# Optimization experiments

Measured on AMD Instinct MI355X. Metric: run time of the kernel, lower is better.

## Reference

```python
import jax, jax.numpy as jnp
import numpy as np

PATCH = 16
CH = 3


def setup_inputs() -> dict:
    key = jax.random.key(0)
    k1, k2, k3 = jax.random.split(key, 3)
    B, H = 16, 512
    embed_dim = PATCH * PATCH * CH  # 768
    x = jax.random.normal(k1, (B, CH, H, H), dtype=jnp.float32)
    fan_in = CH * PATCH * PATCH
    w = jax.random.normal(k2, (embed_dim, CH, PATCH, PATCH), dtype=jnp.float32) / np.float32(np.sqrt(fan_in))
    b = jax.random.normal(k3, (embed_dim,), dtype=jnp.float32) * 0.01
    return {"x": x, "w": w, "b": b}


def reference(x, w, b):
    p = w.shape[2]                      # patch_size
    B, C, imgsize, _ = x.shape
    pn = imgsize // p                   # patch_num (NOTE: pre-padding count, as in source)
    # zero-pad by one patch on every side
    xp = jnp.pad(x, ((0, 0), (0, 0), (p, p), (p, p)))
    # strided patch-embed conv: [B, embed_dim, pn+2, pn+2]
    xt = jax.lax.conv_general_dilated(xp, w, window_strides=(p, p), padding='VALID')
    xt = xt + b[None, :, None, None]
    B1, C1, H1, W1 = xt.shape           # H1 = W1 = pn + 2
    xt = xt.reshape(B1, C1, H1 * W1)
    # same (buggy-looking but faithful) index set / stride-pn neighbors as the source
    idxs = jnp.array([i * pn + j for i in range(1, pn - 1) for j in range(1, pn)], dtype=jnp.int32)
    inv8 = jnp.float32(1.0 / 8.0)

    def body(buf, idx):
        # torch aliases x_final=x_temp, so reads see earlier in-place writes -> sequential scan
        s = (buf[:, :, idx - pn] + buf[:, :, idx + pn]
             + buf[:, :, idx - 1] + buf[:, :, idx + 1]
             + buf[:, :, idx - pn - 1] + buf[:, :, idx - pn + 1]
             + buf[:, :, idx + pn - 1] + buf[:, :, idx + pn + 1]) * inv8
        return buf.at[:, :, idx].set(s), None

    xf, _ = jax.lax.scan(body, xt, idxs)
    side = imgsize + 2 * p              # embed_dim*H1*W1 == C*side*side by construction
    out = xf.reshape(B1, C, side, side)
    return out[:, :, p:imgsize + p, p:imgsize + p]
```

## Files before the change

### kernel.cpp

```cpp
#include <hip/hip_runtime.h>
#include <hip/hip_bf16.h>


typedef __attribute__((ext_vector_type(8))) short s8v;
typedef __attribute__((ext_vector_type(4))) float f4v;
typedef __attribute__((ext_vector_type(8))) unsigned short us8;
typedef __attribute__((ext_vector_type(4))) unsigned short us4;

__device__ __forceinline__ unsigned short f2bf(float f) {
    __hip_bfloat16 h = __float2bfloat16(f);
    return *reinterpret_cast<unsigned short*>(&h);
}
__device__ __forceinline__ float bf2f(unsigned short u) {
    union { unsigned int i; float f; } c; c.i = (unsigned int)u << 16; return c.f;
}

__device__ __forceinline__ void gload_lds16(const void* g, void* l) {
    __builtin_amdgcn_global_load_lds(
        (const __attribute__((address_space(1))) unsigned int*)g,
        (__attribute__((address_space(3))) unsigned int*)l,
        16, 0, 0);
}

__global__ __launch_bounds__(256) void prep_w_k(const float* __restrict__ w,
                                                unsigned short* __restrict__ w_bf) {
    int g = blockIdx.x * 256 + threadIdx.x;
    int f = g << 3;
    const float4 v0 = *(const float4*)(w + f);
    const float4 v1 = *(const float4*)(w + f + 4);
    us8 u;
    u[0] = f2bf(v0.x); u[1] = f2bf(v0.y); u[2] = f2bf(v0.z); u[3] = f2bf(v0.w);
    u[4] = f2bf(v1.x); u[5] = f2bf(v1.y); u[6] = f2bf(v1.z); u[7] = f2bf(v1.w);
    *(us8*)(w_bf + f) = u;
}

__global__ __launch_bounds__(256) void conv_gemm_fused_k(const float* __restrict__ x,
                                                         const unsigned short* __restrict__ W,
                                                         const float* __restrict__ bias,
                                                         unsigned short* __restrict__ xt) {
    __shared__ __align__(16) unsigned short As[2][128 * 32];
    __shared__ __align__(16) unsigned short Bs[2][128 * 32];
    const int tid  = threadIdx.x;
    const int lane = tid & 63, wv = tid >> 6;
    const int wr = wv >> 1, wc = wv & 1;
    const int m0 = blockIdx.x << 7, n0 = blockIdx.y << 7;

    f4v acc[4][4] = {};

    const int bb  = m0 >> 10;
    const int ph0 = (m0 >> 5) & 31;
    const int h_l = tid >> 5, pw = tid & 31;
    const int ph_l = h_l >> 1, py_l = h_l & 1;
    const int arow = (ph_l << 5) + pw;
    const int axr  = (arow >> 1) & 3;
    const int aoff0 = arow * 32 + ((( py_l << 1)      ^ axr) << 3);
    const int aoff1 = arow * 32 + ((((py_l << 1) | 1) ^ axr) << 3);
    const float* asrc = x + (size_t)bb * 786432
                          + ((ph0 + ph_l) * 16 + py_l) * 512 + (pw << 4);
    float4 ar0, ar1, ar2, ar3;
    auto loadA = [&](int k0) {
        const float* s = asrc + (k0 >> 8) * 262144 + ((k0 >> 4) & 15) * 512;
        ar0 = *(const float4*)(s);      ar1 = *(const float4*)(s + 4);
        ar2 = *(const float4*)(s + 8);  ar3 = *(const float4*)(s + 12);
    };
    auto writeA = [&](int buf) {
        us8 lo, hi;
        lo[0]=f2bf(ar0.x); lo[1]=f2bf(ar0.y); lo[2]=f2bf(ar0.z); lo[3]=f2bf(ar0.w);
        lo[4]=f2bf(ar1.x); lo[5]=f2bf(ar1.y); lo[6]=f2bf(ar1.z); lo[7]=f2bf(ar1.w);
        hi[0]=f2bf(ar2.x); hi[1]=f2bf(ar2.y); hi[2]=f2bf(ar2.z); hi[3]=f2bf(ar2.w);
        hi[4]=f2bf(ar3.x); hi[5]=f2bf(ar3.y); hi[6]=f2bf(ar3.z); hi[7]=f2bf(ar3.w);
        *(us8*)(As[buf] + aoff0) = lo;
        *(us8*)(As[buf] + aoff1) = hi;
    };

    const int l2 = lane >> 2;
    const int kx = ((lane & 3) ^ ((l2 >> 1) & 3)) << 3;
    const unsigned short* gB = W + (size_t)(n0 + (wv << 5) + l2) * 768 + kx;
    auto stageB = [&](int buf, int k0) {
        gload_lds16(gB + k0,            Bs[buf] + (wv << 10));
        gload_lds16(gB + k0 + 16 * 768, Bs[buf] + (wv << 10) + 512);
    };

    stageB(0, 0);
    loadA(0);
    writeA(0);
    __syncthreads();

    const int cq = lane >> 4;
    int cur = 0;
    for (int t = 0; t < 24; ++t) {
        if (t < 23) { stageB(cur ^ 1, (t + 1) << 5); loadA((t + 1) << 5); }
        s8v a[4], b[4];
        #pragma unroll
        for (int mi = 0; mi < 4; ++mi) {
            int ra = (wr << 6) + (mi << 4) + (lane & 15);
            a[mi] = *(const s8v*)(As[cur] + (ra << 5) + ((cq ^ ((ra >> 1) & 3)) << 3));
        }
        #pragma unroll
        for (int ni = 0; ni < 4; ++ni) {
            int rb = (wc << 6) + (ni << 4) + (lane & 15);
            b[ni] = *(const s8v*)(Bs[cur] + (rb << 5) + ((cq ^ ((rb >> 1) & 3)) << 3));
        }
        #pragma unroll
        for (int mi = 0; mi < 4; ++mi)
            #pragma unroll
            for (int ni = 0; ni < 4; ++ni)
                acc[mi][ni] = __builtin_amdgcn_mfma_f32_16x16x32_bf16(a[mi], b[ni], acc[mi][ni], 0, 0, 0);
        if (t < 23) writeA(cur ^ 1);
        __syncthreads();
        cur ^= 1;
    }

    #pragma unroll
    for (int mi = 0; mi < 4; ++mi) {
        int m  = m0 + (wr << 6) + (mi << 4) + ((lane >> 4) << 2);
        int ph = (m >> 5) & 31, pwm = m & 31;
        unsigned short* dst = xt + (((size_t)bb * 768) << 10) + (ph << 5) + pwm;
        #pragma unroll
        for (int ni = 0; ni < 4; ++ni) {
            int n = n0 + (wc << 6) + (ni << 4) + (lane & 15);
            float bv = bias[n];
            us4 o;
            o[0] = f2bf(acc[mi][ni][0] + bv);
            o[1] = f2bf(acc[mi][ni][1] + bv);
            o[2] = f2bf(acc[mi][ni][2] + bv);
            o[3] = f2bf(acc[mi][ni][3] + bv);
            *(us4*)(dst + ((size_t)n << 10)) = o;
        }
    }
}

__global__ __launch_bounds__(256) void scan_emit_k(const unsigned short* __restrict__ xt,
                                                   const float* __restrict__ bias,
                                                   float* __restrict__ out) {
    const int grp = (blockIdx.x * 256 + threadIdx.x) >> 5;
    const int j   = threadIdx.x & 31;
    const int b   = grp / 768;
    const int c1  = grp - b * 768;
    const unsigned short* basep = xt + ((size_t)grp << 10);
    float* outb = out + (size_t)b * 786432;
    const int fl0 = c1 * 1156;
    const float bias_c = bias[c1];

    auto emit = [&](int fl, float v) {
        unsigned int c   = (fl >= 591872) ? 2u : (fl >= 295936 ? 1u : 0u);
        unsigned int rem = (unsigned int)fl - c * 295936u;
        unsigned int y   = rem / 544u;
        unsigned int xx  = rem - y * 544u;
        if (y >= 16u && y < 528u && xx >= 16u && xx < 528u)
            outb[(size_t)c * 262144 + (y - 16) * 512 + (xx - 16)] = v;
    };
    auto sel = [&](int p) -> float {
        unsigned int h = (unsigned int)p / 34u;
        unsigned int w = (unsigned int)p - h * 34u;
        if ((h == 0u) | (h == 33u) | (w == 0u) | (w == 33u)) return bias_c;
        return bf2f(basep[(h - 1u) * 32u + (w - 1u)]);
    };

    float co = sel( 32 + j);
    float no = sel( 64 + j);
    float o2 = sel( 96 + j);
    float o3 = sel(128 + j);
    emit(fl0 + j, bias_c);
    float pn   = bias_c;
    float po_h = bias_c;

    for (int i = 1; i <= 30; ++i) {
        float ld = sel((i + 4) * 32 + j);
        float co_head = __shfl(co, 0, 32);
        float no_head = __shfl(no, 0, 32);
        float n2_head = __shfl(o2, 0, 32);
        float UL = __shfl_up(pn, 1, 32);   if (j == 1)  UL = po_h;
        float U  = pn;
        float UR = __shfl_down(pn, 1, 32); if (j == 31) UR = co_head;
        float Rr = __shfl_down(co, 1, 32); if (j == 31) Rr = no_head;
        float D1 = __shfl_up(no, 1, 32);
        float D2 = no;
        float D3 = __shfl_down(no, 1, 32); if (j == 31) D3 = n2_head;
        float bv = (((UL + U) + (UR + Rr)) + ((D1 + D2) + D3)) * 0.125f;
        if (j == 1) bv += co_head * 0.125f;
        float t;
        t = __shfl_up(bv, 1, 32);  bv += (j > 1) ? 0.125f * t : 0.f;
        t = __shfl_up(bv, 2, 32);  bv += (j > 2) ? 0.015625f * t : 0.f;
        t = __shfl_up(bv, 4, 32);  bv += (j > 4) ? 2.44140625e-4f * t : 0.f;
        emit(fl0 + i * 32 + j, (j == 0) ? co : bv);
        pn   = bv;
        po_h = co_head;
        co = no; no = o2; o2 = o3; o3 = ld;
    }
    emit(fl0 +  992 + j, co);
    emit(fl0 + 1024 + j, no);
    emit(fl0 + 1056 + j, o2);
    emit(fl0 + 1088 + j, o3);
    emit(fl0 + 1120 + j, sel(1120 + j));
    if (j < 4) emit(fl0 + 1152 + j, bias_c);
}

extern "C" void kernel_launch(void* const* d_in, const int* in_sizes, int n_in,
                              void* d_out, int out_size, void* d_ws, size_t ws_size,
                              hipStream_t stream) {
    const float* x    = (const float*)d_in[0];
    const float* w    = (const float*)d_in[1];
    const float* bias = (const float*)d_in[2];
    float* out = (float*)d_out;
    unsigned short* xt = (unsigned short*)d_ws;

    unsigned short* w_bf = (unsigned short*)d_out;

    prep_w_k<<<288, 256, 0, stream>>>(w, w_bf);
    conv_gemm_fused_k<<<dim3(128, 6), 256, 0, stream>>>(x, w_bf, bias, xt);
    scan_emit_k<<<1536, 256, 0, stream>>>(xt, bias, out);
}
```

Before: 81.88 us.

## Load GEMM operands directly from global into registers, dropping LDS staging

The conv-GEMM kernel stops staging A and B tiles through shared memory with barriers. Each lane now loads its own MFMA fragments straight from global memory into registers, double-buffered in registers, and converts x to bf16 in registers. This removes LDS traffic and __syncthreads. In exchange, each wave re-reads data that LDS used to share between the wave pair, which raises global/L2 traffic and register pressure.

```diff
diff --git a/kernel.cpp b/kernel.cpp
--- a/kernel.cpp
+++ b/kernel.cpp
@@ -15,13 +15,6 @@
     union { unsigned int i; float f; } c; c.i = (unsigned int)u << 16; return c.f;
 }
 
-__device__ __forceinline__ void gload_lds16(const void* g, void* l) {
-    __builtin_amdgcn_global_load_lds(
-        (const __attribute__((address_space(1))) unsigned int*)g,
-        (__attribute__((address_space(3))) unsigned int*)l,
-        16, 0, 0);
-}
-
 __global__ __launch_bounds__(256) void prep_w_k(const float* __restrict__ w,
                                                 unsigned short* __restrict__ w_bf) {
     int g = blockIdx.x * 256 + threadIdx.x;
@@ -34,91 +27,84 @@
     *(us8*)(w_bf + f) = u;
 }
 
-__global__ __launch_bounds__(256) void conv_gemm_fused_k(const float* __restrict__ x,
-                                                         const unsigned short* __restrict__ W,
-                                                         const float* __restrict__ bias,
-                                                         unsigned short* __restrict__ xt) {
-    __shared__ __align__(16) unsigned short As[2][128 * 32];
-    __shared__ __align__(16) unsigned short Bs[2][128 * 32];
+__global__ __launch_bounds__(256) void conv_gemm_direct_k(const float* __restrict__ x,
+                                                          const unsigned short* __restrict__ W,
+                                                          const float* __restrict__ bias,
+                                                          unsigned short* __restrict__ xt) {
     const int tid  = threadIdx.x;
     const int lane = tid & 63, wv = tid >> 6;
     const int wr = wv >> 1, wc = wv & 1;
     const int m0 = blockIdx.x << 7, n0 = blockIdx.y << 7;
+    const int l15 = lane & 15, chunk = lane >> 4;
+    const int bb = m0 >> 10;
 
     f4v acc[4][4] = {};
 
-    const int bb  = m0 >> 10;
-    const int ph0 = (m0 >> 5) & 31;
-    const int h_l = tid >> 5, pw = tid & 31;
-    const int ph_l = h_l >> 1, py_l = h_l & 1;
-    const int arow = (ph_l << 5) + pw;
-    const int axr  = (arow >> 1) & 3;
-    const int aoff0 = arow * 32 + ((( py_l << 1)      ^ axr) << 3);
-    const int aoff1 = arow * 32 + ((((py_l << 1) | 1) ^ axr) << 3);
-    const float* asrc = x + (size_t)bb * 786432
-                          + ((ph0 + ph_l) * 16 + py_l) * 512 + (pw << 4);
-    float4 ar0, ar1, ar2, ar3;
-    auto loadA = [&](int k0) {
-        const float* s = asrc + (k0 >> 8) * 262144 + ((k0 >> 4) & 15) * 512;
-        ar0 = *(const float4*)(s);      ar1 = *(const float4*)(s + 4);
-        ar2 = *(const float4*)(s + 8);  ar3 = *(const float4*)(s + 12);
-    };
-    auto writeA = [&](int buf) {
-        us8 lo, hi;
-        lo[0]=f2bf(ar0.x); lo[1]=f2bf(ar0.y); lo[2]=f2bf(ar0.z); lo[3]=f2bf(ar0.w);
-        lo[4]=f2bf(ar1.x); lo[5]=f2bf(ar1.y); lo[6]=f2bf(ar1.z); lo[7]=f2bf(ar1.w);
-        hi[0]=f2bf(ar2.x); hi[1]=f2bf(ar2.y); hi[2]=f2bf(ar2.z); hi[3]=f2bf(ar2.w);
-        hi[4]=f2bf(ar3.x); hi[5]=f2bf(ar3.y); hi[6]=f2bf(ar3.z); hi[7]=f2bf(ar3.w);
-        *(us8*)(As[buf] + aoff0) = lo;
-        *(us8*)(As[buf] + aoff1) = hi;
-    };
+    const float* xb[4];
+    #pragma unroll
+    for (int mi = 0; mi < 4; ++mi) {
+        int m  = m0 + (wr << 6) + (mi << 4) + l15;
+        int pw = m & 31, ph = (m >> 5) & 31;
+        xb[mi] = x + (size_t)bb * 786432 + ph * 8192 + (pw << 4)
+               + (chunk >> 1) * 512 + ((chunk & 1) << 3);
+    }
+    const unsigned short* wb[4];
+    #pragma unroll
+    for (int ni = 0; ni < 4; ++ni)
+        wb[ni] = W + (size_t)(n0 + (wc << 6) + (ni << 4) + l15) * 768 + (chunk << 3);
 
-    const int l2 = lane >> 2;
-    const int kx = ((lane & 3) ^ ((l2 >> 1) & 3)) << 3;
-    const unsigned short* gB = W + (size_t)(n0 + (wv << 5) + l2) * 768 + kx;
-    auto stageB = [&](int buf, int k0) {
-        gload_lds16(gB + k0,            Bs[buf] + (wv << 10));
-        gload_lds16(gB + k0 + 16 * 768, Bs[buf] + (wv << 10) + 512);
-    };
+    float4 xr[2][4][2];
+    s8v    wf[2][4];
 
-    stageB(0, 0);
-    loadA(0);
-    writeA(0);
-    __syncthreads();
+#define XLOAD(P, T)                                                          \
+    {                                                                        \
+        int ko = ((T) >> 3) * 262144 + ((T) & 7) * 1024;                     \
+        int wo = (T) << 5;                                                   \
+        _Pragma("unroll")                                                    \
+        for (int mi = 0; mi < 4; ++mi) {                                     \
+            xr[P][mi][0] = *(const float4*)(xb[mi] + ko);                    \
+            xr[P][mi][1] = *(const float4*)(xb[mi] + ko + 4);                \
+        }                                                                    \
+        _Pragma("unroll")                                                    \
+        for (int ni = 0; ni < 4; ++ni)                                       \
+            wf[P][ni] = *(const s8v*)(wb[ni] + wo);                          \
+    }
 
-    const int cq = lane >> 4;
-    int cur = 0;
+    XLOAD(0, 0);
+    #pragma unroll
     for (int t = 0; t < 24; ++t) {
-        if (t < 23) { stageB(cur ^ 1, (t + 1) << 5); loadA((t + 1) << 5); }
-        s8v a[4], b[4];
+        const int p = t & 1;
+        if (t < 23) XLOAD(p ^ 1, t + 1);
+        s8v a[4];
         #pragma unroll
         for (int mi = 0; mi < 4; ++mi) {
-            int ra = (wr << 6) + (mi << 4) + (lane & 15);
-            a[mi] = *(const s8v*)(As[cur] + (ra << 5) + ((cq ^ ((ra >> 1) & 3)) << 3));
-        }
-        #pragma unroll
-        for (int ni = 0; ni < 4; ++ni) {
-            int rb = (wc << 6) + (ni << 4) + (lane & 15);
-            b[ni] = *(const s8v*)(Bs[cur] + (rb << 5) + ((cq ^ ((rb >> 1) & 3)) << 3));
+            s8v av;
+            av[0] = (short)f2bf(xr[p][mi][0].x);
+            av[1] = (short)f2bf(xr[p][mi][0].y);
+            av[2] = (short)f2bf(xr[p][mi][0].z);
+            av[3] = (short)f2bf(xr[p][mi][0].w);
+            av[4] = (short)f2bf(xr[p][mi][1].x);
+            av[5] = (short)f2bf(xr[p][mi][1].y);
+            av[6] = (short)f2bf(xr[p][mi][1].z);
+            av[7] = (short)f2bf(xr[p][mi][1].w);
+            a[mi] = av;
         }
         #pragma unroll
         for (int mi = 0; mi < 4; ++mi)
             #pragma unroll
             for (int ni = 0; ni < 4; ++ni)
-                acc[mi][ni] = __builtin_amdgcn_mfma_f32_16x16x32_bf16(a[mi], b[ni], acc[mi][ni], 0, 0, 0);
-        if (t < 23) writeA(cur ^ 1);
-        __syncthreads();
-        cur ^= 1;
+                acc[mi][ni] = __builtin_amdgcn_mfma_f32_16x16x32_bf16(a[mi], wf[p][ni], acc[mi][ni], 0, 0, 0);
     }
+#undef XLOAD
 
     #pragma unroll
     for (int mi = 0; mi < 4; ++mi) {
-        int m  = m0 + (wr << 6) + (mi << 4) + ((lane >> 4) << 2);
+        int m  = m0 + (wr << 6) + (mi << 4) + (chunk << 2);
         int ph = (m >> 5) & 31, pwm = m & 31;
         unsigned short* dst = xt + (((size_t)bb * 768) << 10) + (ph << 5) + pwm;
         #pragma unroll
         for (int ni = 0; ni < 4; ++ni) {
-            int n = n0 + (wc << 6) + (ni << 4) + (lane & 15);
+            int n = n0 + (wc << 6) + (ni << 4) + l15;
             float bv = bias[n];
             us4 o;
             o[0] = f2bf(acc[mi][ni][0] + bv);
@@ -208,6 +194,6 @@
     unsigned short* w_bf = (unsigned short*)d_out;
 
     prep_w_k<<<288, 256, 0, stream>>>(w, w_bf);
-    conv_gemm_fused_k<<<dim3(128, 6), 256, 0, stream>>>(x, w_bf, bias, xt);
+    conv_gemm_direct_k<<<dim3(128, 6), 256, 0, stream>>>(x, w_bf, bias, xt);
     scan_emit_k<<<1536, 256, 0, stream>>>(xt, bias, out);
 }
```

Measured after the change: 123.0 us. 50.2% more time.
